# Kernel tuning notes

Measured on AMD Instinct MI355X. Metric: run time of the kernel, lower is better.

Reference implementation:

```python
import jax, jax.numpy as jnp
import numpy as np

B, T, C = 4, 4096, 256
H = 4
D = C // H
EPS = 1e-5


def layer_norm(x, w, b):
    mean = x.mean(axis=-1, keepdims=True)
    var = x.var(axis=-1, keepdims=True)
    return w * (x - mean) / jnp.sqrt(var + EPS) + b


def setup_inputs() -> dict:
    key = jax.random.key(0)
    ks = jax.random.split(key, 8)
    s = lambda n: 1.0 / np.sqrt(n)
    return {
        "x": jax.random.normal(ks[0], (B, T, C), jnp.float32),
        "qkv_w": jax.random.normal(ks[1], (C, 3 * C), jnp.float32) * s(C),
        "qkv_b": jnp.zeros((3 * C,), jnp.float32),
        "proj_w": jax.random.normal(ks[2], (C, C), jnp.float32) * s(C),
        "proj_b": jnp.zeros((C,), jnp.float32),
        "n1_w": jnp.ones((C,), jnp.float32),
        "n1_b": jnp.zeros((C,), jnp.float32),
        "ffn_w1": jax.random.normal(ks[3], (C, 3 * C), jnp.float32) * s(C),
        "ffn_b1": jnp.zeros((3 * C,), jnp.float32),
        "ffn_w2": jax.random.normal(ks[4], (3 * C, C), jnp.float32) * s(3 * C),
        "ffn_b2": jnp.zeros((C,), jnp.float32),
        "n2_w": jnp.ones((C,), jnp.float32),
        "n2_b": jnp.zeros((C,), jnp.float32),
    }


def reference(x, qkv_w, qkv_b, proj_w, proj_b, n1_w, n1_b,
              ffn_w1, ffn_b1, ffn_w2, ffn_b2, n2_w, n2_b):
    scale = D ** -0.5
    qkv = (x @ qkv_w + qkv_b).reshape(B, T, 3, H, D)
    qkv = jnp.transpose(qkv, (2, 0, 3, 1, 4))  # [3, B, H, T, D]
    q, k, v = qkv[0], qkv[1], qkv[2]
    attn = jnp.einsum('bhtd,bhsd->bhts', q, k) * scale  # [B,H,T,T]
    attn = jax.nn.softmax(attn, axis=-1)
    out = jnp.einsum('bhts,bhsd->bhtd', attn, v)
    out = jnp.transpose(out, (0, 2, 1, 3)).reshape(B, T, C)
    attn_out = out @ proj_w + proj_b
    x = layer_norm(x + attn_out, n1_w, n1_b)
    h = jax.nn.gelu(x @ ffn_w1 + ffn_b1, approximate=False)
    ffn_out = h @ ffn_w2 + ffn_b2
    x = layer_norm(x + ffn_out, n2_w, n2_b)
    return x
```

## Files before the change

### kernel.cpp

```cpp
#include <hip/hip_runtime.h>
#include <cstdint>
#include <cstddef>

typedef __bf16 bf16;
typedef __bf16 bf16x8 __attribute__((ext_vector_type(8)));
typedef __bf16 bf16x4 __attribute__((ext_vector_type(4)));
typedef _Float16 f16;
typedef _Float16 f16x4 __attribute__((ext_vector_type(4)));
typedef _Float16 f16x8 __attribute__((ext_vector_type(8)));
typedef __fp16 fp16x2 __attribute__((ext_vector_type(2)));
typedef float f32x4 __attribute__((ext_vector_type(4)));

#define DEV static __device__ __forceinline__
#if __has_builtin(__builtin_amdgcn_exp2f)
#define EXP2(x) __builtin_amdgcn_exp2f(x)
#else
#define EXP2(x) exp2f(x)
#endif
#define QSCALE 0.18033688011112042f

DEV float gelu_exact(float v) {
  return 0.5f * v * (1.0f + erff(v * 0.70710678118654752f));
}

template <int ROWS>
DEV void stage_swz(bf16* lbase, const bf16* g, int ldK) {
  const int tid = threadIdx.x;
  const int wave = tid >> 6, lane = tid & 63;
  const int r8 = lane >> 3;
  const int c = (lane & 7) ^ r8;
  const size_t goff = (size_t)r8 * ldK + c * 8;
#pragma unroll
  for (int ch = wave; ch < (ROWS >> 3); ch += 4) {
    __builtin_amdgcn_global_load_lds(
        (const __attribute__((address_space(1))) void*)(g + (size_t)ch * 8 * ldK + goff),
        (__attribute__((address_space(3))) void*)(lbase + ch * 512), 16, 0, 0);
  }
}

DEV int swzi(int R, int c) { return R * 64 + ((c ^ (R & 7)) << 3); }

__global__ void cvt_w_kernel(const float* __restrict__ qkv_w, bf16* __restrict__ qwt,
                             const float* __restrict__ proj_w, bf16* __restrict__ pwt,
                             const float* __restrict__ f1w, bf16* __restrict__ f1wt,
                             const float* __restrict__ f2w, bf16* __restrict__ f2wt,
                             const float* __restrict__ x, bf16* __restrict__ xb) {
  int blk = blockIdx.x;
  const int tid = threadIdx.x;
  if (blk >= 160) {
    const size_t i = ((size_t)(blk - 160) * 256 + tid) * 8;
    const float4 a0 = *(const float4*)(x + i);
    const float4 a1 = *(const float4*)(x + i + 4);
    bf16x8 v;
    v[0] = (bf16)a0.x; v[1] = (bf16)a0.y; v[2] = (bf16)a0.z; v[3] = (bf16)a0.w;
    v[4] = (bf16)a1.x; v[5] = (bf16)a1.y; v[6] = (bf16)a1.z; v[7] = (bf16)a1.w;
    *(bf16x8*)(xb + i) = v;
    return;
  }
  const float* w; bf16* o; int K, N;
  if (blk < 48)       { w = qkv_w;  o = qwt;  K = 256; N = 768; }
  else if (blk < 64)  { w = proj_w; o = pwt;  K = 256; N = 256; blk -= 48; }
  else if (blk < 112) { w = f1w;    o = f1wt; K = 256; N = 768; blk -= 64; }
  else                { w = f2w;    o = f2wt; K = 768; N = 256; blk -= 112; }
  const int ntiles = N >> 6;
  const int kt = blk / ntiles, nt = blk - kt * ntiles;
  const int k0 = kt * 64, n0 = nt * 64;
  __shared__ float tile[64][65];
#pragma unroll
  for (int j = 0; j < 4; ++j) {
    const int c = j * 256 + tid;
    const int row = c >> 4, c4 = (c & 15) * 4;
    const float4 v = *(const float4*)(w + (size_t)(k0 + row) * N + n0 + c4);
    tile[row][c4] = v.x; tile[row][c4 + 1] = v.y;
    tile[row][c4 + 2] = v.z; tile[row][c4 + 3] = v.w;
  }
  __syncthreads();
#pragma unroll
  for (int j = 0; j < 4; ++j) {
    const int c = j * 256 + tid;
    const int n = c >> 4, k4 = (c & 15) * 4;
    bf16x4 ov;
#pragma unroll
    for (int i = 0; i < 4; ++i) ov[i] = (bf16)tile[k4 + i][n];
    *(bf16x4*)(o + (size_t)(n0 + n) * K + k0 + k4) = ov;
  }
}

__global__ __launch_bounds__(256, 3)
void gemm_qkv_kernel(const bf16* __restrict__ A, const bf16* __restrict__ Wt,
                     const float* __restrict__ bias, bf16* __restrict__ qb,
                     bf16* __restrict__ kb, f16* __restrict__ vt) {
  const int tid = threadIdx.x;
  const int wave = tid >> 6, lane = tid & 63;
  const int quad = lane >> 4, l15 = lane & 15;
  const int m0 = blockIdx.y * 128, n0 = blockIdx.x * 128;
  const int mw = (wave >> 1) * 64, nw = (wave & 1) * 64;
  const int K = 256;

  __shared__ __align__(16) char smem[128 * 132 * 2];
  bf16* lA = (bf16*)smem;
  bf16* lB = lA + 128 * 64;

  f32x4 acc[4][4] = {};

  for (int k0 = 0; k0 < K; k0 += 64) {
    stage_swz<128>(lA, A + (size_t)m0 * K + k0, K);
    stage_swz<128>(lB, Wt + (size_t)n0 * K + k0, K);
    __syncthreads();
#pragma unroll
    for (int ks = 0; ks < 2; ++ks) {
      bf16x8 af[4], bfm[4];
#pragma unroll
      for (int i = 0; i < 4; ++i)
        af[i] = *(const bf16x8*)(lA + swzi(mw + i * 16 + l15, ks * 4 + quad));
#pragma unroll
      for (int j = 0; j < 4; ++j)
        bfm[j] = *(const bf16x8*)(lB + swzi(nw + j * 16 + l15, ks * 4 + quad));
#pragma unroll
      for (int i = 0; i < 4; ++i)
#pragma unroll
        for (int j = 0; j < 4; ++j)
          acc[i][j] = __builtin_amdgcn_mfma_f32_16x16x32_bf16(af[i], bfm[j],
                                                              acc[i][j], 0, 0, 0);
    }
    __syncthreads();
  }

  const int b = m0 >> 12, trow = m0 & 4095;
  const bool isV = (n0 >= 512);
  float bv[4];
#pragma unroll
  for (int j = 0; j < 4; ++j) bv[j] = bias[n0 + nw + 16 * j + l15];

  if (isV) {
    f16* ET = (f16*)smem;
#pragma unroll
    for (int i = 0; i < 4; ++i)
#pragma unroll
      for (int j = 0; j < 4; ++j) {
        const int n = nw + 16 * j + l15, t = mw + 16 * i + quad * 4;
        f16x4 hv;
#pragma unroll
        for (int r = 0; r < 4; ++r) hv[r] = (f16)(acc[i][j][r] + bv[j]);
        *(f16x4*)(ET + n * 132 + t) = hv;
      }
    __syncthreads();
    const int nr = tid >> 4, l4 = tid & 15;
    const int g32 = l4 >> 2, q8 = l4 & 3;
#pragma unroll
    for (int pass = 0; pass < 8; ++pass) {
      const int n = pass * 16 + nr;
      const int gn = n0 + n;
      const int h = (gn >> 6) & 3, d = gn & 63;
      const f16* srcr = ET + n * 132 + g32 * 32 + q8 * 4;
      const f16x4 lo = *(const f16x4*)(srcr);
      const f16x4 hi = *(const f16x4*)(srcr + 16);
      union { f16x4 h4[2]; f16x8 h8; } u;
      u.h4[0] = lo; u.h4[1] = hi;
      *(f16x8*)(vt + ((size_t)(b * 4 + h) * 64 + d) * 4096 + trow + l4 * 8) =
          u.h8;
    }
  } else {
    const bool isQ = (n0 < 256);
    const float sc = isQ ? QSCALE : 1.0f;
    bf16* ET = (bf16*)smem;
#pragma unroll
    for (int i = 0; i < 4; ++i)
#pragma unroll
      for (int j = 0; j < 4; ++j) {
        const int n = nw + 16 * j + l15;
#pragma unroll
        for (int r = 0; r < 4; ++r) {
          const int t = mw + 16 * i + quad * 4 + r;
          ET[t * 132 + n] = (bf16)((acc[i][j][r] + bv[j]) * sc);
        }
      }
    __syncthreads();
    bf16* qk = isQ ? qb : kb;
    const int nr = tid >> 4, l4 = tid & 15;
    const int gn = n0 + l4 * 8;
    const int h = (gn >> 6) & 3, d = gn & 63;
#pragma unroll
    for (int pass = 0; pass < 8; ++pass) {
      const int t = pass * 16 + nr;
      const bf16x4 lo = *(const bf16x4*)(ET + t * 132 + l4 * 8);
      const bf16x4 hi = *(const bf16x4*)(ET + t * 132 + l4 * 8 + 4);
      union { bf16x4 h4[2]; bf16x8 h8; } u;
      u.h4[0] = lo; u.h4[1] = hi;
      *(bf16x8*)(qk + ((size_t)(b * 4 + h) * 4096 + trow + t) * 64 + d) = u.h8;
    }
  }
}

__global__ __launch_bounds__(256, 2)
void attn_kernel(const bf16* __restrict__ q, const bf16* __restrict__ k,
                 const f16* __restrict__ vt, bf16* __restrict__ o0,
                 bf16* __restrict__ o1, float* __restrict__ pD) {
  const int tid = threadIdx.x;
  const int wave = tid >> 6, lane = tid & 63;
  const int quad = lane >> 4, l15 = lane & 15;
  const int bh = blockIdx.y;
  const int q0 = blockIdx.x * 128;
  const int z = blockIdx.z;
  const int kvbase = z * 2048;
  __shared__ bf16 lK[2][64 * 64];
  __shared__ f16  lV[2][64 * 64];

  bf16x8 qa0[2], qa1[2];
#pragma unroll
  for (int s = 0; s < 2; ++s) {
    const bf16* qp =
        q + ((size_t)bh * 4096 + q0 + wave * 32 + s * 16 + l15) * 64 + quad * 8;
    qa0[s] = *(const bf16x8*)(qp);
    qa1[s] = *(const bf16x8*)(qp + 32);
  }

  const int srow = lane >> 3;
  const int sc = (lane & 7) ^ srow;
  const bf16* kbase = k + ((size_t)bh * 4096 + kvbase) * 64;
  const f16*  vbase = vt + (size_t)bh * 64 * 4096 + kvbase;

#define STAGE_KV(buf, it_)                                                     \
  {                                                                            \
    const bf16* ks_ = kbase + (size_t)(it_) * 4096;                            \
    const f16*  vs_ = vbase + (it_) * 64;                                      \
    _Pragma("unroll")                                                          \
    for (int i_ = 0; i_ < 2; ++i_) {                                           \
      const int r0_ = i_ * 32 + wave * 8;                                      \
      __builtin_amdgcn_global_load_lds(                                        \
          (const __attribute__((address_space(1))) void*)(                     \
              ks_ + (size_t)(r0_ + srow) * 64 + sc * 8),                       \
          (__attribute__((address_space(3))) void*)(lK[buf] + r0_ * 64),       \
          16, 0, 0);                                                           \
      __builtin_amdgcn_global_load_lds(                                        \
          (const __attribute__((address_space(1))) void*)(                     \
              vs_ + (size_t)(r0_ + srow) * 4096 + sc * 8),                     \
          (__attribute__((address_space(3))) void*)(lV[buf] + r0_ * 64),       \
          16, 0, 0);                                                           \
    }                                                                          \
  }

  STAGE_KV(0, 0);

  f32x4 accO[2][4] = {};
  f32x4 accD[2] = {};
  const f16x8 vone8 = {(f16)1.0f, (f16)1.0f, (f16)1.0f, (f16)1.0f,
                       (f16)1.0f, (f16)1.0f, (f16)1.0f, (f16)1.0f};

  for (int it = 0; it < 32; ++it) {
    const int cur = it & 1;
    __syncthreads();
    if (it + 1 < 32) STAGE_KV(cur ^ 1, it + 1);

    f32x4 sf[2][4];
    __builtin_amdgcn_s_setprio(1);
#pragma unroll
    for (int c = 0; c < 4; ++c) {
      const bf16x8 kb0 = *(const bf16x8*)(lK[cur] + swzi(c * 16 + l15, quad));
      const bf16x8 kb1 = *(const bf16x8*)(lK[cur] + swzi(c * 16 + l15, 4 + quad));
#pragma unroll
      for (int s = 0; s < 2; ++s) {
        f32x4 t = {};
        t = __builtin_amdgcn_mfma_f32_16x16x32_bf16(kb0, qa0[s], t, 0, 0, 0);
        t = __builtin_amdgcn_mfma_f32_16x16x32_bf16(kb1, qa1[s], t, 0, 0, 0);
        sf[s][c] = t;
      }
    }
    __builtin_amdgcn_s_setprio(0);

    f16x8 pa[2][2];
#pragma unroll
    for (int s = 0; s < 2; ++s)
#pragma unroll
      for (int c2 = 0; c2 < 2; ++c2) {
        union { fp16x2 h2[4]; f16x8 h8; } u;
        u.h2[0] = __builtin_amdgcn_cvt_pkrtz(EXP2(sf[s][2 * c2][0]),
                                             EXP2(sf[s][2 * c2][1]));
        u.h2[1] = __builtin_amdgcn_cvt_pkrtz(EXP2(sf[s][2 * c2][2]),
                                             EXP2(sf[s][2 * c2][3]));
        u.h2[2] = __builtin_amdgcn_cvt_pkrtz(EXP2(sf[s][2 * c2 + 1][0]),
                                             EXP2(sf[s][2 * c2 + 1][1]));
        u.h2[3] = __builtin_amdgcn_cvt_pkrtz(EXP2(sf[s][2 * c2 + 1][2]),
                                             EXP2(sf[s][2 * c2 + 1][3]));
        pa[s][c2] = u.h8;
      }

    __builtin_amdgcn_s_setprio(1);
#pragma unroll
    for (int s = 0; s < 2; ++s)
#pragma unroll
      for (int c2 = 0; c2 < 2; ++c2)
        accD[s] = __builtin_amdgcn_mfma_f32_16x16x32_f16(pa[s][c2], vone8,
                                                         accD[s], 0, 0, 0);

#pragma unroll
    for (int c2 = 0; c2 < 2; ++c2) {
#pragma unroll
      for (int n = 0; n < 4; ++n) {
        const f16x8 vb =
            *(const f16x8*)(lV[cur] + swzi(n * 16 + l15, c2 * 4 + quad));
#pragma unroll
        for (int s = 0; s < 2; ++s)
          accO[s][n] = __builtin_amdgcn_mfma_f32_16x16x32_f16(pa[s][c2], vb,
                                                              accO[s][n], 0, 0, 0);
      }
    }
    __builtin_amdgcn_s_setprio(0);
  }
#undef STAGE_KV

  bf16* po = z ? o1 : o0;
  const int b = bh >> 2, h = bh & 3;
#pragma unroll
  for (int s = 0; s < 2; ++s) {
    float inv[4];
#pragma unroll
    for (int r = 0; r < 4; ++r) inv[r] = 1.0f / accD[s][r];
#pragma unroll
    for (int r = 0; r < 4; ++r) {
      const int t = q0 + wave * 32 + s * 16 + quad * 4 + r;
      if (l15 == 0) pD[(size_t)(z * 16 + bh) * 4096 + t] = accD[s][r];
#pragma unroll
      for (int n = 0; n < 4; ++n)
        po[(size_t)(b * 4096 + t) * 256 + h * 64 + n * 16 + l15] =
            (bf16)(accO[s][n][r] * inv[r]);
    }
  }
}

__global__ __launch_bounds__(256, 2)
void ln1_ffn1_kernel(const bf16* __restrict__ A, const bf16* __restrict__ A2,
                     const float* __restrict__ pD, const bf16* __restrict__ pwt,
                     const float* __restrict__ pb, const float* __restrict__ xres,
                     const float* __restrict__ lw, const float* __restrict__ lb,
                     bf16* __restrict__ x1b, const bf16* __restrict__ f1wt,
                     const float* __restrict__ f1b, bf16* __restrict__ ob) {
  const int tid = threadIdx.x;
  const int wave = tid >> 6, lane = tid & 63;
  const int quad = lane >> 4, l15 = lane & 15;
  const int m0 = blockIdx.x * 32;
  const int nw = wave * 64;
  __shared__ bf16 lA[32 * 64];
  __shared__ bf16 lB[256 * 64];
  __shared__ bf16 aT[4 * 32 * 64];
  __shared__ float lnsum[4][32];
  __shared__ float lnsq[4][32];
  __shared__ float lnstat[32][2];
  f32x4 acc[2][4] = {};

  for (int kt = 0; kt < 4; ++kt) {
    const int k0 = kt * 64;
    {
      const int row = tid >> 3, cc = tid & 7;
      const int am = m0 + row;
      const int ab = am >> 12, at = am & 4095;
      const float d0 = pD[(size_t)(ab * 4 + kt) * 4096 + at];
      const float d1 = pD[(size_t)(16 + ab * 4 + kt) * 4096 + at];
      const float wsum = 1.0f / (d0 + d1);
      const float w0 = d0 * wsum, w1 = d1 * wsum;
      const bf16x8 a0 = *(const bf16x8*)(A  + (size_t)am * 256 + k0 + cc * 8);
      const bf16x8 a1 = *(const bf16x8*)(A2 + (size_t)am * 256 + k0 + cc * 8);
      bf16x8 cv;
#pragma unroll
      for (int i = 0; i < 8; ++i)
        cv[i] = (bf16)((float)a0[i] * w0 + (float)a1[i] * w1);
      *(bf16x8*)(lA + swzi(row, cc)) = cv;
    }
    stage_swz<256>(lB, pwt + k0, 256);
    __syncthreads();
#pragma unroll
    for (int ks = 0; ks < 2; ++ks) {
      bf16x8 af[2], bfm[4];
#pragma unroll
      for (int i = 0; i < 2; ++i)
        af[i] = *(const bf16x8*)(lA + swzi(i * 16 + l15, ks * 4 + quad));
#pragma unroll
      for (int j = 0; j < 4; ++j)
        bfm[j] = *(const bf16x8*)(lB + swzi(nw + j * 16 + l15, ks * 4 + quad));
#pragma unroll
      for (int i = 0; i < 2; ++i)
#pragma unroll
        for (int j = 0; j < 4; ++j)
          acc[i][j] = __builtin_amdgcn_mfma_f32_16x16x32_bf16(af[i], bfm[j],
                                                              acc[i][j], 0, 0, 0);
    }
    __syncthreads();
  }

  float bv[4], lwv[4], lbv[4];
#pragma unroll
  for (int j = 0; j < 4; ++j) {
    const int col = nw + 16 * j + l15;
    bv[j] = pb[col]; lwv[j] = lw[col]; lbv[j] = lb[col];
  }
#pragma unroll
  for (int i = 0; i < 2; ++i) {
    float ps[4] = {}, pq[4] = {};
#pragma unroll
    for (int j = 0; j < 4; ++j) {
#pragma unroll
      for (int r = 0; r < 4; ++r) {
        const int m = m0 + 16 * i + 4 * quad + r;
        const size_t ri = (size_t)m * 256 + nw + 16 * j + l15;
        const float v = acc[i][j][r] + bv[j] + xres[ri];
        acc[i][j][r] = v;
        ps[r] += v;
        pq[r] += v * v;
      }
    }
#pragma unroll
    for (int r = 0; r < 4; ++r) {
#pragma unroll
      for (int mm = 1; mm < 16; mm <<= 1) {
        ps[r] += __shfl_xor(ps[r], mm, 64);
        pq[r] += __shfl_xor(pq[r], mm, 64);
      }
      if (l15 == 0) {
        lnsum[wave][16 * i + 4 * quad + r] = ps[r];
        lnsq[wave][16 * i + 4 * quad + r] = pq[r];
      }
    }
  }
  __syncthreads();
  if (tid < 32) {
    const float s = lnsum[0][tid] + lnsum[1][tid] + lnsum[2][tid] + lnsum[3][tid];
    const float sq = lnsq[0][tid] + lnsq[1][tid] + lnsq[2][tid] + lnsq[3][tid];
    const float mean = s * (1.0f / 256.0f);
    const float var = sq * (1.0f / 256.0f) - mean * mean;
    lnstat[tid][0] = mean;
    lnstat[tid][1] = rsqrtf(var + 1e-5f);
  }
  __syncthreads();
#pragma unroll
  for (int i = 0; i < 2; ++i) {
#pragma unroll
    for (int r = 0; r < 4; ++r) {
      const int row = 16 * i + 4 * quad + r;
      const float mean = lnstat[row][0], rstd = lnstat[row][1];
#pragma unroll
      for (int j = 0; j < 4; ++j) {
        const float ov = (acc[i][j][r] - mean) * rstd * lwv[j] + lbv[j];
        const bf16 obf = (bf16)ov;
        const size_t gi = (size_t)(m0 + row) * 256 + nw + 16 * j + l15;
        x1b[gi] = obf;
        const int cg = 16 * j + l15;
        aT[wave * 2048 + row * 64 + ((((cg >> 3) ^ (row & 7))) << 3) + (cg & 7)]
            = obf;
      }
    }
  }
  __syncthreads();

  const int nwB = wave * 32;
#pragma unroll 1
  for (int nt = 0; nt < 6; ++nt) {
    f32x4 acc2[2][2] = {};
    const bf16* Bb = f1wt + (size_t)nt * 128 * 256;
#pragma unroll 1
    for (int kh = 0; kh < 2; ++kh) {
      stage_swz<128>(lB,        Bb + kh * 128, 256);
      stage_swz<128>(lB + 8192, Bb + kh * 128 + 64, 256);
      __syncthreads();
#pragma unroll
      for (int kk = 0; kk < 2; ++kk) {
        const bf16* aTk = aT + (kh * 2 + kk) * 2048;
        const bf16* lbk = lB + kk * 8192;
#pragma unroll
        for (int ks = 0; ks < 2; ++ks) {
          bf16x8 af[2], bfm[2];
#pragma unroll
          for (int i = 0; i < 2; ++i)
            af[i] = *(const bf16x8*)(aTk + swzi(i * 16 + l15, ks * 4 + quad));
#pragma unroll
          for (int j = 0; j < 2; ++j)
            bfm[j] = *(const bf16x8*)(lbk + swzi(nwB + j * 16 + l15, ks * 4 + quad));
#pragma unroll
          for (int i = 0; i < 2; ++i)
#pragma unroll
            for (int j = 0; j < 2; ++j)
              acc2[i][j] = __builtin_amdgcn_mfma_f32_16x16x32_bf16(
                  af[i], bfm[j], acc2[i][j], 0, 0, 0);
        }
      }
      __syncthreads();
    }
#pragma unroll
    for (int j = 0; j < 2; ++j) {
      const int gn = nt * 128 + nwB + 16 * j + l15;
      const float bs = f1b[gn];
#pragma unroll
      for (int i = 0; i < 2; ++i)
#pragma unroll
        for (int r = 0; r < 4; ++r) {
          const int m = m0 + 16 * i + quad * 4 + r;
          ob[(size_t)m * 768 + gn] = (bf16)gelu_exact(acc2[i][j][r] + bs);
        }
    }
  }
}

template <int KTILES, bool RESID_BF16, bool WRITE_F, bool WRITE_B>
__global__ __launch_bounds__(256, 3)
void gemm_ln_kernel(const bf16* __restrict__ A, const bf16* __restrict__ Wt,
                    const float* __restrict__ bias, const void* __restrict__ Rv,
                    const float* __restrict__ lw, const float* __restrict__ lb,
                    float* __restrict__ outf, bf16* __restrict__ outb) {
  const int tid = threadIdx.x;
  const int wave = tid >> 6, lane = tid & 63;
  const int quad = lane >> 4, l15 = lane & 15;
  const int m0 = blockIdx.x * 32;
  const int nw = wave * 64;
  const int K = KTILES * 64;
  __shared__ bf16 lA[32 * 64];
  __shared__ bf16 lB[256 * 64];
  __shared__ float lnsum[4][32];
  __shared__ float lnsq[4][32];
  __shared__ float lnstat[32][2];
  f32x4 acc[2][4] = {};

  for (int kt = 0; kt < KTILES; ++kt) {
    const int k0 = kt * 64;
    stage_swz<32>(lA, A + (size_t)m0 * K + k0, K);
    stage_swz<256>(lB, Wt + k0, K);
    __syncthreads();
#pragma unroll
    for (int ks = 0; ks < 2; ++ks) {
      bf16x8 af[2], bfm[4];
#pragma unroll
      for (int i = 0; i < 2; ++i)
        af[i] = *(const bf16x8*)(lA + swzi(i * 16 + l15, ks * 4 + quad));
#pragma unroll
      for (int j = 0; j < 4; ++j)
        bfm[j] = *(const bf16x8*)(lB + swzi(nw + j * 16 + l15, ks * 4 + quad));
#pragma unroll
      for (int i = 0; i < 2; ++i)
#pragma unroll
        for (int j = 0; j < 4; ++j)
          acc[i][j] = __builtin_amdgcn_mfma_f32_16x16x32_bf16(af[i], bfm[j],
                                                              acc[i][j], 0, 0, 0);
    }
    __syncthreads();
  }

  float bv[4], lwv[4], lbv[4];
#pragma unroll
  for (int j = 0; j < 4; ++j) {
    const int col = nw + 16 * j + l15;
    bv[j] = bias[col]; lwv[j] = lw[col]; lbv[j] = lb[col];
  }
#pragma unroll
  for (int i = 0; i < 2; ++i) {
    float ps[4] = {}, pq[4] = {};
#pragma unroll
    for (int j = 0; j < 4; ++j) {
#pragma unroll
      for (int r = 0; r < 4; ++r) {
        const int m = m0 + 16 * i + 4 * quad + r;
        const size_t ri = (size_t)m * 256 + nw + 16 * j + l15;
        const float rv = RESID_BF16 ? (float)((const bf16*)Rv)[ri]
                                    : ((const float*)Rv)[ri];
        const float v = acc[i][j][r] + bv[j] + rv;
        acc[i][j][r] = v;
        ps[r] += v;
        pq[r] += v * v;
      }
    }
#pragma unroll
    for (int r = 0; r < 4; ++r) {
#pragma unroll
      for (int mm = 1; mm < 16; mm <<= 1) {
        ps[r] += __shfl_xor(ps[r], mm, 64);
        pq[r] += __shfl_xor(pq[r], mm, 64);
      }
      if (l15 == 0) {
        lnsum[wave][16 * i + 4 * quad + r] = ps[r];
        lnsq[wave][16 * i + 4 * quad + r] = pq[r];
      }
    }
  }
  __syncthreads();
  if (tid < 32) {
    const float s = lnsum[0][tid] + lnsum[1][tid] + lnsum[2][tid] + lnsum[3][tid];
    const float sq = lnsq[0][tid] + lnsq[1][tid] + lnsq[2][tid] + lnsq[3][tid];
    const float mean = s * (1.0f / 256.0f);
    const float var = sq * (1.0f / 256.0f) - mean * mean;
    lnstat[tid][0] = mean;
    lnstat[tid][1] = rsqrtf(var + 1e-5f);
  }
  __syncthreads();
#pragma unroll
  for (int i = 0; i < 2; ++i) {
#pragma unroll
    for (int r = 0; r < 4; ++r) {
      const int row = 16 * i + 4 * quad + r;
      const float mean = lnstat[row][0], rstd = lnstat[row][1];
#pragma unroll
      for (int j = 0; j < 4; ++j) {
        const float ov = (acc[i][j][r] - mean) * rstd * lwv[j] + lbv[j];
        const size_t gi = (size_t)(m0 + row) * 256 + nw + 16 * j + l15;
        if constexpr (WRITE_F) outf[gi] = ov;
        if constexpr (WRITE_B) outb[gi] = (bf16)ov;
      }
    }
  }
}

extern "C" void kernel_launch(void* const* d_in, const int* in_sizes, int n_in,
                              void* d_out, int out_size, void* d_ws, size_t ws_size,
                              hipStream_t stream) {
  const float* x      = (const float*)d_in[0];
  const float* qkv_w  = (const float*)d_in[1];
  const float* qkv_b  = (const float*)d_in[2];
  const float* proj_w = (const float*)d_in[3];
  const float* proj_b = (const float*)d_in[4];
  const float* n1_w   = (const float*)d_in[5];
  const float* n1_b   = (const float*)d_in[6];
  const float* ffn_w1 = (const float*)d_in[7];
  const float* ffn_b1 = (const float*)d_in[8];
  const float* ffn_w2 = (const float*)d_in[9];
  const float* ffn_b2 = (const float*)d_in[10];
  const float* n2_w   = (const float*)d_in[11];
  const float* n2_b   = (const float*)d_in[12];
  float* out = (float*)d_out;

  char* ws = (char*)d_ws;
  bf16*  qwt  = (bf16*)(ws + 0);
  bf16*  pwt  = (bf16*)(ws + 393216);
  bf16*  f1wt = (bf16*)(ws + 524288);
  bf16*  f2wt = (bf16*)(ws + 917504);
  bf16*  qb   = (bf16*)(ws + 1310720);
  bf16*  kb   = (bf16*)(ws + 9699328);
  f16*   vtb  = (f16*)(ws + 18087936);
  bf16*  attn = (bf16*)(ws + 26476544);
  bf16*  x1b  = (bf16*)(ws + 34865152);
  bf16*  hbuf = (bf16*)(ws + 1310720);
  bf16*  xb   = (bf16*)(ws + 34865152);
  bf16*  po1  = (bf16*)(ws + 43253760);
  float* pden = (float*)(ws + 51642368);

  cvt_w_kernel<<<2208, 256, 0, stream>>>(qkv_w, qwt, proj_w, pwt,
                                         ffn_w1, f1wt, ffn_w2, f2wt, x, xb);
  gemm_qkv_kernel<<<dim3(6, 128), 256, 0, stream>>>(xb, qwt, qkv_b, qb, kb, vtb);
  attn_kernel<<<dim3(32, 16, 2), 256, 0, stream>>>(qb, kb, vtb, attn, po1, pden);
  ln1_ffn1_kernel<<<512, 256, 0, stream>>>(attn, po1, pden, pwt, proj_b, x,
                                           n1_w, n1_b, x1b, f1wt, ffn_b1, hbuf);
  gemm_ln_kernel<12, true, true, false><<<512, 256, 0, stream>>>(
      hbuf, f2wt, ffn_b2, x1b, n2_w, n2_b, out, nullptr);
}
```

Measured before the change: 227.2 us.

## Double-buffer LDS staging in FFN1 and GEMM+LN kernels

Both the fused LN+FFN1 loop and the gemm_ln kernel now use two shared-memory buffers. The next K-tile is staged while the current one is consumed, which removes one barrier per iteration and lets global loads overlap with MFMA work. The gemm_ln kernel doubles its LDS footprint, so its launch bounds drop from 3 to 2 blocks per CU, costing occupancy. The FFN1 loop is flattened into 24 steps that each stage a single 64-wide slice.

```diff
diff --git a/kernel.cpp b/kernel.cpp
--- a/kernel.cpp
+++ b/kernel.cpp
@@ -452,55 +452,61 @@
   __syncthreads();
 
   const int nwB = wave * 32;
+  f32x4 acc2[2][2] = {};
+  stage_swz<128>(lB, f1wt, 256);
 #pragma unroll 1
-  for (int nt = 0; nt < 6; ++nt) {
-    f32x4 acc2[2][2] = {};
-    const bf16* Bb = f1wt + (size_t)nt * 128 * 256;
-#pragma unroll 1
-    for (int kh = 0; kh < 2; ++kh) {
-      stage_swz<128>(lB,        Bb + kh * 128, 256);
-      stage_swz<128>(lB + 8192, Bb + kh * 128 + 64, 256);
-      __syncthreads();
-#pragma unroll
-      for (int kk = 0; kk < 2; ++kk) {
-        const bf16* aTk = aT + (kh * 2 + kk) * 2048;
-        const bf16* lbk = lB + kk * 8192;
-#pragma unroll
-        for (int ks = 0; ks < 2; ++ks) {
-          bf16x8 af[2], bfm[2];
-#pragma unroll
-          for (int i = 0; i < 2; ++i)
-            af[i] = *(const bf16x8*)(aTk + swzi(i * 16 + l15, ks * 4 + quad));
-#pragma unroll
-          for (int j = 0; j < 2; ++j)
-            bfm[j] = *(const bf16x8*)(lbk + swzi(nwB + j * 16 + l15, ks * 4 + quad));
-#pragma unroll
-          for (int i = 0; i < 2; ++i)
-#pragma unroll
-            for (int j = 0; j < 2; ++j)
-              acc2[i][j] = __builtin_amdgcn_mfma_f32_16x16x32_bf16(
-                  af[i], bfm[j], acc2[i][j], 0, 0, 0);
-        }
-      }
-      __syncthreads();
-    }
-#pragma unroll
-    for (int j = 0; j < 2; ++j) {
-      const int gn = nt * 128 + nwB + 16 * j + l15;
-      const float bs = f1b[gn];
+  for (int u = 0; u < 24; ++u) {
+    const int cur = u & 1;
+    __syncthreads();
+    if (u + 1 < 24) {
+      const int un = u + 1;
+      const int ntn = un >> 2, khn = (un >> 1) & 1, kkn = un & 1;
+      stage_swz<128>((un & 1) ? lB + 8192 : lB,
+                     f1wt + (size_t)ntn * 128 * 256 + khn * 128 + kkn * 64, 256);
+    }
+    const int kh = (u >> 1) & 1, kk = u & 1;
+    const bf16* aTk = aT + (kh * 2 + kk) * 2048;
+    const bf16* lbk = cur ? lB + 8192 : lB;
+#pragma unroll
+    for (int ks = 0; ks < 2; ++ks) {
+      bf16x8 af[2], bfm[2];
 #pragma unroll
       for (int i = 0; i < 2; ++i)
-#pragma unroll
-        for (int r = 0; r < 4; ++r) {
-          const int m = m0 + 16 * i + quad * 4 + r;
-          ob[(size_t)m * 768 + gn] = (bf16)gelu_exact(acc2[i][j][r] + bs);
-        }
+        af[i] = *(const bf16x8*)(aTk + swzi(i * 16 + l15, ks * 4 + quad));
+#pragma unroll
+      for (int j = 0; j < 2; ++j)
+        bfm[j] = *(const bf16x8*)(lbk + swzi(nwB + j * 16 + l15, ks * 4 + quad));
+#pragma unroll
+      for (int i = 0; i < 2; ++i)
+#pragma unroll
+        for (int j = 0; j < 2; ++j)
+          acc2[i][j] = __builtin_amdgcn_mfma_f32_16x16x32_bf16(
+              af[i], bfm[j], acc2[i][j], 0, 0, 0);
+    }
+    if ((u & 3) == 3) {
+      const int nt = u >> 2;
+#pragma unroll
+      for (int j = 0; j < 2; ++j) {
+        const int gn = nt * 128 + nwB + 16 * j + l15;
+        const float bs = f1b[gn];
+#pragma unroll
+        for (int i = 0; i < 2; ++i)
+#pragma unroll
+          for (int r = 0; r < 4; ++r) {
+            const int m = m0 + 16 * i + quad * 4 + r;
+            ob[(size_t)m * 768 + gn] = (bf16)gelu_exact(acc2[i][j][r] + bs);
+          }
+      }
+#pragma unroll
+      for (int i = 0; i < 2; ++i)
+#pragma unroll
+        for (int j = 0; j < 2; ++j) acc2[i][j] = (f32x4){};
     }
   }
 }
 
 template <int KTILES, bool RESID_BF16, bool WRITE_F, bool WRITE_B>
-__global__ __launch_bounds__(256, 3)
+__global__ __launch_bounds__(256, 2)
 void gemm_ln_kernel(const bf16* __restrict__ A, const bf16* __restrict__ Wt,
                     const float* __restrict__ bias, const void* __restrict__ Rv,
                     const float* __restrict__ lw, const float* __restrict__ lb,
@@ -511,27 +517,33 @@
   const int m0 = blockIdx.x * 32;
   const int nw = wave * 64;
   const int K = KTILES * 64;
-  __shared__ bf16 lA[32 * 64];
-  __shared__ bf16 lB[256 * 64];
+  __shared__ bf16 lA[2][32 * 64];
+  __shared__ bf16 lB[2][256 * 64];
   __shared__ float lnsum[4][32];
   __shared__ float lnsq[4][32];
   __shared__ float lnstat[32][2];
   f32x4 acc[2][4] = {};
 
+  stage_swz<32>(lA[0], A + (size_t)m0 * K, K);
+  stage_swz<256>(lB[0], Wt, K);
+
   for (int kt = 0; kt < KTILES; ++kt) {
-    const int k0 = kt * 64;
-    stage_swz<32>(lA, A + (size_t)m0 * K + k0, K);
-    stage_swz<256>(lB, Wt + k0, K);
-    __syncthreads();
+    const int cur = kt & 1;
+    __syncthreads();
+    if (kt + 1 < KTILES) {
+      const int kn = (kt + 1) * 64;
+      stage_swz<32>(lA[cur ^ 1], A + (size_t)m0 * K + kn, K);
+      stage_swz<256>(lB[cur ^ 1], Wt + kn, K);
+    }
 #pragma unroll
     for (int ks = 0; ks < 2; ++ks) {
       bf16x8 af[2], bfm[4];
 #pragma unroll
       for (int i = 0; i < 2; ++i)
-        af[i] = *(const bf16x8*)(lA + swzi(i * 16 + l15, ks * 4 + quad));
+        af[i] = *(const bf16x8*)(lA[cur] + swzi(i * 16 + l15, ks * 4 + quad));
 #pragma unroll
       for (int j = 0; j < 4; ++j)
-        bfm[j] = *(const bf16x8*)(lB + swzi(nw + j * 16 + l15, ks * 4 + quad));
+        bfm[j] = *(const bf16x8*)(lB[cur] + swzi(nw + j * 16 + l15, ks * 4 + quad));
 #pragma unroll
       for (int i = 0; i < 2; ++i)
 #pragma unroll
@@ -539,7 +551,6 @@
           acc[i][j] = __builtin_amdgcn_mfma_f32_16x16x32_bf16(af[i], bfm[j],
                                                               acc[i][j], 0, 0, 0);
     }
-    __syncthreads();
   }
 
   float bv[4], lwv[4], lbv[4];
```

Measured after the change: 225.5 us. Within noise of the previous version (-0.7%).
